# Optimization experiments

Measured on AMD Instinct MI355X. Metric: run time of the kernel, lower is better.

The kernel has to match this reference:

```python
import jax, jax.numpy as jnp
import numpy as np

N_NODES = 100000
N_EDGES = 1600000
IN_C, HID_C, OUT_C = 128, 128, 64


def setup_inputs() -> dict:
    key = jax.random.key(0)
    ks = jax.random.split(key, 8)
    x = jax.random.normal(ks[0], (N_NODES, IN_C), dtype=jnp.float32)
    edge_index = jax.random.randint(ks[1], (2, N_EDGES), 0, N_NODES, dtype=jnp.int32)
    # Glorot-ish init for GCNConv linear weights, zero bias (PyG default)
    def glorot(k, fan_in, fan_out):
        s = jnp.sqrt(6.0 / (fan_in + fan_out))
        return jax.random.uniform(k, (fan_in, fan_out), dtype=jnp.float32, minval=-s, maxval=s)
    return {
        "x": x,
        "edge_index": edge_index,
        "W1": glorot(ks[2], IN_C, HID_C), "b1": jnp.zeros((HID_C,), jnp.float32),
        "W2": glorot(ks[3], HID_C, HID_C), "b2": jnp.zeros((HID_C,), jnp.float32),
        "W3": glorot(ks[4], HID_C, OUT_C), "b3": jnp.zeros((OUT_C,), jnp.float32),
    }


def _gcn_norm(edge_index, num_nodes):
    # Add self-loops (PyG GCNConv default) and compute symmetric normalization
    loops = jnp.arange(num_nodes, dtype=edge_index.dtype)
    src = jnp.concatenate([edge_index[0], loops])  # [E+N]
    dst = jnp.concatenate([edge_index[1], loops])
    deg = jax.ops.segment_sum(jnp.ones_like(dst, dtype=jnp.float32), dst,
                              num_segments=num_nodes)
    deg_inv_sqrt = jnp.where(deg > 0, jax.lax.rsqrt(jnp.maximum(deg, 1.0)), 0.0)
    norm = deg_inv_sqrt[src] * deg_inv_sqrt[dst]  # [E+N]
    return src, dst, norm


def _gcn_layer(x, src, dst, norm, W, b, num_nodes):
    h = x @ W                                # [N, out] dense transform first
    msg = h[src] * norm[:, None]             # gather + scale  [E+N, out]
    out = jax.ops.segment_sum(msg, dst, num_segments=num_nodes)  # scatter-add
    return out + b


def reference(x, edge_index, W1, b1, W2, b2, W3, b3):
    n = x.shape[0]
    src, dst, norm = _gcn_norm(edge_index, n)
    h = jax.nn.relu(_gcn_layer(x, src, dst, norm, W1, b1, n))
    h = jax.nn.relu(_gcn_layer(h, src, dst, norm, W2, b2, n))
    return _gcn_layer(h, src, dst, norm, W3, b3, n)
```

## Files before the change

kernel.cpp:

```cpp
#include <hip/hip_runtime.h>

#define NN 100000
#define NE 1600000
#define NBK 391
#define BSH 8
#define MPAD 100096
#define SCB 391
#define CAP 5120

typedef unsigned short ushortT;
typedef unsigned long long ull;
using sh8 = __attribute__((ext_vector_type(8))) short;
using f4  = __attribute__((ext_vector_type(4))) float;


__device__ __forceinline__ unsigned short bfr(float f) {
  unsigned u = __float_as_uint(f);
  u += 0x7FFF + ((u >> 16) & 1);
  return (unsigned short)(u >> 16);
}
__device__ __forceinline__ float bf2f(unsigned short h) {
  return __uint_as_float(((unsigned)h) << 16);
}
__device__ __forceinline__ void acc8(const uint4 v, float* a) {
  a[0] += __uint_as_float(v.x << 16);
  a[1] += __uint_as_float(v.x & 0xFFFF0000u);
  a[2] += __uint_as_float(v.y << 16);
  a[3] += __uint_as_float(v.y & 0xFFFF0000u);
  a[4] += __uint_as_float(v.z << 16);
  a[5] += __uint_as_float(v.z & 0xFFFF0000u);
  a[6] += __uint_as_float(v.w << 16);
  a[7] += __uint_as_float(v.w & 0xFFFF0000u);
}
__device__ __forceinline__ sh8 hi8(const float4 a, const float4 b) {
  sh8 r;
  r[0] = (short)bfr(a.x); r[1] = (short)bfr(a.y);
  r[2] = (short)bfr(a.z); r[3] = (short)bfr(a.w);
  r[4] = (short)bfr(b.x); r[5] = (short)bfr(b.y);
  r[6] = (short)bfr(b.z); r[7] = (short)bfr(b.w);
  return r;
}


template <int COUT>
__device__ __forceinline__ void packone(const float* __restrict__ W,
                                        ushortT* __restrict__ Bp, int i) {
  const int j = i & 7;
  const int l = (i >> 3) & 63;
  const int rest = i >> 9;
  const int g = rest % (COUT / 16);
  const int ks = rest / (COUT / 16);
  const int k = (ks & 3) * 32 + (l >> 4) * 8 + j;
  const int n = g * 16 + (l & 15);
  const float v = W[k * COUT + n];
  const unsigned short h = bfr(v);
  Bp[i] = (ks < 4) ? h : bfr(v - bf2f(h));
}


__global__ __launch_bounds__(256) void k_scatterpack(
    const int* __restrict__ src, const int* __restrict__ dst,
    int* __restrict__ cursor, unsigned* __restrict__ pairArr,
    const float* __restrict__ W1, const float* __restrict__ W2,
    const float* __restrict__ W3, ushortT* __restrict__ Bp1,
    ushortT* __restrict__ Bp2, ushortT* __restrict__ Bp3) {
  if (blockIdx.x >= SCB) {
    const int i = (blockIdx.x - SCB) * 256 + threadIdx.x;
    if (i < 32768) packone<128>(W1, Bp1, i);
    else if (i < 65536) packone<128>(W2, Bp2, i - 32768);
    else packone<64>(W3, Bp3, i - 65536);
    return;
  }
  __shared__ int lcnt[512];
  __shared__ int lbase[512];
  __shared__ int lrank[NBK];
  __shared__ int bbase[NBK];
  __shared__ int sd2[256];
  __shared__ unsigned sorted[4096];
  __shared__ int target[4096];
  const int t = threadIdx.x;
  for (int i = t; i < 512; i += 256) lcnt[i] = 0;
  for (int i = t; i < NBK; i += 256) lrank[i] = 0;
  __syncthreads();
  const int base = blockIdx.x * 4096;
  int rs[16], rd[16];
#pragma unroll
  for (int q = 0; q < 16; q++) {
    int e = base + t + 256 * q;
    rs[q] = (e < NE) ? src[e] : -1;
    rd[q] = (e < NE) ? dst[e] : -1;
    if (rd[q] >= 0) atomicAdd(&lcnt[rd[q] >> BSH], 1);
  }
  __syncthreads();
  const int s0 = lcnt[2 * t];
  const int s1 = lcnt[2 * t + 1];
  sd2[t] = s0 + s1;
  __syncthreads();
  for (int off = 1; off < 256; off <<= 1) {
    int x = (t >= off) ? sd2[t - off] : 0;
    __syncthreads();
    sd2[t] += x;
    __syncthreads();
  }
  const int epair = sd2[t] - (s0 + s1);
  lbase[2 * t] = epair;
  lbase[2 * t + 1] = epair + s0;
  __syncthreads();
  for (int i = t; i < NBK; i += 256)
    if (lcnt[i] > 0) bbase[i] = atomicAdd(&cursor[i], lcnt[i]);
  __syncthreads();
#pragma unroll
  for (int q = 0; q < 16; q++) {
    if (rd[q] >= 0) {
      int b = rd[q] >> BSH;
      int r = atomicAdd(&lrank[b], 1);
      int slot = lbase[b] + r;
      sorted[slot] = ((unsigned)rs[q] << 8) | ((unsigned)rd[q] & 255u);
      target[slot] = b * CAP + bbase[b] + r;
    }
  }
  __syncthreads();
  const int n = min(4096, NE - base);
  for (int s = t; s < n; s += 256) pairArr[target[s]] = sorted[s];
}


__global__ __launch_bounds__(256) void k_buildcsr(const unsigned* __restrict__ pairArr,
                                                  const int* __restrict__ cnt,
                                                  float* __restrict__ dinv,
                                                  int* __restrict__ rowptr,
                                                  int* __restrict__ col) {
  __shared__ int lc[256];
  __shared__ int sd[256];
  __shared__ int bc[NBK];
  const int t = threadIdx.x;
  const int b = blockIdx.x;
  const int n0 = b << BSH;
  for (int i = t; i < NBK; i += 256) bc[i] = cnt[i];
  lc[t] = 0;
  __syncthreads();
  int partial = 0;
  for (int i = t; i < b; i += 256) partial += bc[i];
  sd[t] = partial;
  __syncthreads();
  for (int off = 128; off > 0; off >>= 1) {
    if (t < off) sd[t] += sd[t + off];
    __syncthreads();
  }
  const int ebeg = sd[0];
  const int myCnt = bc[b];
  __syncthreads();
  const unsigned* pb = pairArr + (size_t)b * CAP;
  for (int i = t; i < myCnt; i += 256)
    atomicAdd(&lc[pb[i] & 255u], 1);
  __syncthreads();
  const int v = lc[t];
  sd[t] = v;
  __syncthreads();
  for (int off = 1; off < 256; off <<= 1) {
    int x = (t >= off) ? sd[t - off] : 0;
    __syncthreads();
    sd[t] += x;
    __syncthreads();
  }
  const int excl = sd[t] - v;
  lc[t] = excl;
  const int node = n0 + t;
  if (node < NN) {
    rowptr[node] = ebeg + excl;
    dinv[node] = rsqrtf(1.0f + (float)v);
  }
  if (b == 0 && t == 0) rowptr[NN] = NE;
  __syncthreads();
  for (int i = t; i < myCnt; i += 256) {
    unsigned p = pb[i];
    int d = (int)(p & 255u);
    int srcv = (int)(p >> 8);
    int pos = atomicAdd(&lc[d], 1);
    col[ebeg + pos] = srcv;
  }
}


template <int COUT, bool FUSED>
__global__ __launch_bounds__(256) void k_gemmM(const ushortT* __restrict__ A,
                                               const float* __restrict__ X,
                                               const ushortT* __restrict__ Bp,
                                               const float* __restrict__ dinv,
                                               ushortT* __restrict__ hs) {
  constexpr int CGALL = COUT / 16;
  constexpr int RG = 2;
  constexpr int CG = 4;
  const int w = threadIdx.x >> 6;
  const int lane = threadIdx.x & 63;
  const int q = lane >> 4;
  const int c = lane & 15;
  int row0, cg0;
  if (COUT == 128) {
    row0 = blockIdx.x * 64 + (w & 1) * 32;
    cg0 = (w >> 1) * 4;
  } else {
    row0 = blockIdx.x * 128 + w * 32;
    cg0 = 0;
  }

  const ushortT* ap[RG];
  const float* xp[RG];
#pragma unroll
  for (int rg = 0; rg < RG; rg++) {
    const int row = row0 + rg * 16 + c;
    if (FUSED) xp[rg] = X + (size_t)min(row, NN - 1) * 128 + q * 8;
    else ap[rg] = A + (size_t)row * 128 + q * 8;
  }
  const ushortT* bp0 = Bp + (size_t)lane * 8;

  f4 acc[RG][CG];
#pragma unroll
  for (int i = 0; i < RG; i++)
#pragma unroll
    for (int j = 0; j < CG; j++) acc[i][j] = (f4){0.f, 0.f, 0.f, 0.f};

  sh8 ah[RG], bh[CG], bl[CG];
  sh8 nah[RG], nbh[CG], nbl[CG];

  auto loadA = [&](int kr, sh8 (&h)[RG]) {
#pragma unroll
    for (int rg = 0; rg < RG; rg++) {
      if (FUSED) {
        const float4 x0 = *reinterpret_cast<const float4*>(xp[rg] + kr * 32);
        const float4 x1 = *reinterpret_cast<const float4*>(xp[rg] + kr * 32 + 4);
        h[rg] = hi8(x0, x1);
      } else {
        h[rg] = *reinterpret_cast<const sh8*>(ap[rg] + kr * 32);
      }
    }
  };
  auto loadB = [&](int kr, sh8 (&h)[CG], sh8 (&l)[CG]) {
#pragma unroll
    for (int cg = 0; cg < CG; cg++) {
      h[cg] = *reinterpret_cast<const sh8*>(bp0 + (size_t)(kr * CGALL + cg0 + cg) * 512);
      l[cg] = *reinterpret_cast<const sh8*>(bp0 + (size_t)((4 + kr) * CGALL + cg0 + cg) * 512);
    }
  };

  loadA(0, ah);
  loadB(0, bh, bl);
#pragma unroll
  for (int kr = 0; kr < 4; kr++) {
    if (kr < 3) {
      loadA(kr + 1, nah);
      loadB(kr + 1, nbh, nbl);
    }
#pragma unroll
    for (int rg = 0; rg < RG; rg++)
#pragma unroll
      for (int cg = 0; cg < CG; cg++)
        acc[rg][cg] = __builtin_amdgcn_mfma_f32_16x16x32_bf16(ah[rg], bh[cg],
                                                              acc[rg][cg], 0, 0, 0);
#pragma unroll
    for (int rg = 0; rg < RG; rg++)
#pragma unroll
      for (int cg = 0; cg < CG; cg++)
        acc[rg][cg] = __builtin_amdgcn_mfma_f32_16x16x32_bf16(ah[rg], bl[cg],
                                                              acc[rg][cg], 0, 0, 0);
    if (kr < 3) {
#pragma unroll
      for (int rg = 0; rg < RG; rg++) ah[rg] = nah[rg];
#pragma unroll
      for (int cg = 0; cg < CG; cg++) { bh[cg] = nbh[cg]; bl[cg] = nbl[cg]; }
    }
  }

#pragma unroll
  for (int rg = 0; rg < RG; rg++) {
#pragma unroll
    for (int reg = 0; reg < 4; reg++) {
      const int row = row0 + rg * 16 + q * 4 + reg;
      if (row < NN) {
        const float dv = dinv[row];
#pragma unroll
        for (int cg = 0; cg < CG; cg++) {
          hs[(size_t)row * COUT + (cg0 + cg) * 16 + c] = bfr(acc[rg][cg][reg] * dv);
        }
      }
    }
  }
}


template <bool RELU>
__global__ __launch_bounds__(256) void k_agg128(const ushortT* __restrict__ hs,
                                                const int* __restrict__ rowptr,
                                                const int* __restrict__ col,
                                                const float* __restrict__ dinv,
                                                const float* __restrict__ bias,
                                                ushortT* __restrict__ A) {
  const int gid = blockIdx.x * 256 + threadIdx.x;
  const int node = gid >> 6;
  if (node >= NN) return;
  const int lane = threadIdx.x & 63;
  const int q = lane >> 4;
  const int chb = (lane & 15) * 8;
  const int beg = rowptr[node];
  const int end = rowptr[node + 1];

  float a[8] = {};
  if (q == 0) {
    const uint4 v = *reinterpret_cast<const uint4*>(hs + (long)node * 128 + chb);
    acc8(v, a);
  }

  int j = beg;
  if (j + 16 <= end) {
    int c0 = col[j + q];
    int c1 = col[j + 4 + q];
    int c2 = col[j + 8 + q];
    int c3 = col[j + 12 + q];
    while (true) {
      const uint4 v0 = *reinterpret_cast<const uint4*>(hs + (long)c0 * 128 + chb);
      const uint4 v1 = *reinterpret_cast<const uint4*>(hs + (long)c1 * 128 + chb);
      const uint4 v2 = *reinterpret_cast<const uint4*>(hs + (long)c2 * 128 + chb);
      const uint4 v3 = *reinterpret_cast<const uint4*>(hs + (long)c3 * 128 + chb);
      j += 16;
      const bool more = (j + 16 <= end);
      int n0, n1, n2, n3;
      if (more) {
        n0 = col[j + q]; n1 = col[j + 4 + q];
        n2 = col[j + 8 + q]; n3 = col[j + 12 + q];
      }
      acc8(v0, a);
      acc8(v1, a);
      acc8(v2, a);
      acc8(v3, a);
      if (!more) break;
      c0 = n0; c1 = n1; c2 = n2; c3 = n3;
    }
  }
  if (j + 8 <= end) {
    int c0 = col[j + q];
    int c1 = col[j + 4 + q];
    const uint4 v0 = *reinterpret_cast<const uint4*>(hs + (long)c0 * 128 + chb);
    const uint4 v1 = *reinterpret_cast<const uint4*>(hs + (long)c1 * 128 + chb);
    acc8(v0, a);
    acc8(v1, a);
    j += 8;
  }
  if (j + 4 <= end) {
    int c = col[j + q];
    const uint4 v = *reinterpret_cast<const uint4*>(hs + (long)c * 128 + chb);
    acc8(v, a);
    j += 4;
  }
  {
    const int r = end - j;
    if (q < r) {
      int c = col[j + q];
      const uint4 v = *reinterpret_cast<const uint4*>(hs + (long)c * 128 + chb);
      acc8(v, a);
    }
  }

#pragma unroll
  for (int i = 0; i < 8; i++) a[i] += __shfl(a[i], lane ^ 32);
#pragma unroll
  for (int i = 0; i < 8; i++) a[i] += __shfl(a[i], lane ^ 16);

  if (q == 0) {
    const float di = dinv[node];
    const float4 b0 = *reinterpret_cast<const float4*>(bias + chb);
    const float4 b1 = *reinterpret_cast<const float4*>(bias + chb + 4);
    float o[8];
    o[0] = fmaf(a[0], di, b0.x); o[1] = fmaf(a[1], di, b0.y);
    o[2] = fmaf(a[2], di, b0.z); o[3] = fmaf(a[3], di, b0.w);
    o[4] = fmaf(a[4], di, b1.x); o[5] = fmaf(a[5], di, b1.y);
    o[6] = fmaf(a[6], di, b1.z); o[7] = fmaf(a[7], di, b1.w);
    if (RELU) {
#pragma unroll
      for (int i = 0; i < 8; i++) o[i] = fmaxf(o[i], 0.f);
    }
    uint4 H;
    H.x = (unsigned)bfr(o[0]) | ((unsigned)bfr(o[1]) << 16);
    H.y = (unsigned)bfr(o[2]) | ((unsigned)bfr(o[3]) << 16);
    H.z = (unsigned)bfr(o[4]) | ((unsigned)bfr(o[5]) << 16);
    H.w = (unsigned)bfr(o[6]) | ((unsigned)bfr(o[7]) << 16);
    *reinterpret_cast<uint4*>(A + (long)node * 128 + chb) = H;
  }
}

__global__ __launch_bounds__(256) void k_agg64(const ushortT* __restrict__ hs,
                                               const int* __restrict__ rowptr,
                                               const int* __restrict__ col,
                                               const float* __restrict__ dinv,
                                               const float* __restrict__ bias,
                                               float* __restrict__ out) {
  const int gid = blockIdx.x * 256 + threadIdx.x;
  const int node = gid >> 6;
  if (node >= NN) return;
  const int lane = threadIdx.x & 63;
  const int o8 = lane >> 3;
  const int chb = (lane & 7) * 8;
  const int beg = rowptr[node];
  const int end = rowptr[node + 1];

  float a[8] = {};
  if (o8 == 0) {
    const uint4 v = *reinterpret_cast<const uint4*>(hs + (long)node * 64 + chb);
    acc8(v, a);
  }

  int j = beg;
  if (j + 16 <= end) {
    int c0 = col[j + o8];
    int c1 = col[j + 8 + o8];
    while (true) {
      const uint4 v0 = *reinterpret_cast<const uint4*>(hs + (long)c0 * 64 + chb);
      const uint4 v1 = *reinterpret_cast<const uint4*>(hs + (long)c1 * 64 + chb);
      j += 16;
      const bool more = (j + 16 <= end);
      int n0, n1;
      if (more) { n0 = col[j + o8]; n1 = col[j + 8 + o8]; }
      acc8(v0, a);
      acc8(v1, a);
      if (!more) break;
      c0 = n0; c1 = n1;
    }
  }
  for (; j + 8 <= end; j += 8) {
    int c = col[j + o8];
    const uint4 v = *reinterpret_cast<const uint4*>(hs + (long)c * 64 + chb);
    acc8(v, a);
  }
  {
    const int r = end - j;
    if (o8 < r) {
      int c = col[j + o8];
      const uint4 v = *reinterpret_cast<const uint4*>(hs + (long)c * 64 + chb);
      acc8(v, a);
    }
  }

#pragma unroll
  for (int i = 0; i < 8; i++) a[i] += __shfl(a[i], lane ^ 32);
#pragma unroll
  for (int i = 0; i < 8; i++) a[i] += __shfl(a[i], lane ^ 16);
#pragma unroll
  for (int i = 0; i < 8; i++) a[i] += __shfl(a[i], lane ^ 8);

  if (o8 == 0) {
    const float di = dinv[node];
    const float4 b0 = *reinterpret_cast<const float4*>(bias + chb);
    const float4 b1 = *reinterpret_cast<const float4*>(bias + chb + 4);
    float4 r0, r1;
    r0.x = fmaf(a[0], di, b0.x); r0.y = fmaf(a[1], di, b0.y);
    r0.z = fmaf(a[2], di, b0.z); r0.w = fmaf(a[3], di, b0.w);
    r1.x = fmaf(a[4], di, b1.x); r1.y = fmaf(a[5], di, b1.y);
    r1.z = fmaf(a[6], di, b1.z); r1.w = fmaf(a[7], di, b1.w);
    *reinterpret_cast<float4*>(out + (long)node * 64 + chb) = r0;
    *reinterpret_cast<float4*>(out + (long)node * 64 + chb + 4) = r1;
  }
}


extern "C" void kernel_launch(void* const* d_in, const int* in_sizes, int n_in,
                              void* d_out, int out_size, void* d_ws, size_t ws_size,
                              hipStream_t stream) {
  const float* x  = (const float*)d_in[0];
  const int* ei   = (const int*)d_in[1];
  const float* W1 = (const float*)d_in[2];
  const float* b1 = (const float*)d_in[3];
  const float* W2 = (const float*)d_in[4];
  const float* b2 = (const float*)d_in[5];
  const float* W3 = (const float*)d_in[6];
  const float* b3 = (const float*)d_in[7];
  float* out = (float*)d_out;
  const int* srcp = ei;
  const int* dstp = ei + NE;

  char* wsb = (char*)d_ws;
  size_t off = 0;
  auto alloc = [&](size_t bytes) -> void* {
    void* p = wsb + off;
    off += (bytes + 255) & ~(size_t)255;
    return p;
  };
  ushortT* A   = (ushortT*)alloc((size_t)MPAD * 128 * 2);
  ushortT* hs  = (ushortT*)alloc((size_t)NN * 128 * 2);
  int*   col    = (int*)alloc((size_t)NE * 4);
  int*   rowptr = (int*)alloc((size_t)(NN + 1) * 4);
  float* dinv   = (float*)alloc((size_t)NN * 4);
  int*   cursor = (int*)alloc((size_t)NBK * 4);
  ushortT* Bp1 = (ushortT*)alloc((size_t)32768 * 2);
  ushortT* Bp2 = (ushortT*)alloc((size_t)32768 * 2);
  ushortT* Bp3 = (ushortT*)alloc((size_t)16384 * 2);
  unsigned* pairArr = (unsigned*)hs;
  (void)ws_size; (void)in_sizes; (void)n_in; (void)out_size;

  hipMemsetAsync(cursor, 0, (size_t)NBK * 4, stream);
  k_scatterpack<<<SCB + 320, 256, 0, stream>>>(srcp, dstp, cursor, pairArr,
                                               W1, W2, W3, Bp1, Bp2, Bp3);
  k_buildcsr<<<NBK, 256, 0, stream>>>(pairArr, cursor, dinv, rowptr, col);

  const int aggGrid = (NN * 64) / 256;
  const int gemmGrid128 = MPAD / 64;
  const int gemmGrid64 = MPAD / 128;

  k_gemmM<128, true><<<gemmGrid128, 256, 0, stream>>>(nullptr, x, Bp1, dinv, hs);
  k_agg128<true><<<aggGrid, 256, 0, stream>>>(hs, rowptr, col, dinv, b1, A);
  k_gemmM<128, false><<<gemmGrid128, 256, 0, stream>>>(A, nullptr, Bp2, dinv, hs);
  k_agg128<true><<<aggGrid, 256, 0, stream>>>(hs, rowptr, col, dinv, b2, A);
  k_gemmM<64, false><<<gemmGrid64, 256, 0, stream>>>(A, nullptr, Bp3, dinv, hs);
  k_agg64<<<aggGrid, 256, 0, stream>>>(hs, rowptr, col, dinv, b3, out);
}
```

Before: 366.9 us.

## Fuse neighbor aggregation with the next layer's GEMM via shared-memory tile

Replaces the separate aggregation kernel and the following MFMA GEMM with one kernel. Each block aggregates 64 nodes, writes the post-ReLU bf16 rows into a swizzled LDS tile, then multiplies that tile by the packed weights and writes the scaled result. This removes the round trip of the intermediate activation matrix A through global memory and two kernel launches. In exchange, each wave processes 16 nodes serially with a shallower unroll, so latency hiding for the irregular gathers may drop.

Result: slower. 386.7 us (+5.4%).

```diff
diff --git a/kernel.cpp b/kernel.cpp
--- a/kernel.cpp
+++ b/kernel.cpp
@@ -7,6 +7,7 @@
 #define MPAD 100096
 #define SCB 391
 #define CAP 5120
+#define NB64 1563
 
 typedef unsigned short ushortT;
 typedef unsigned long long ull;
@@ -288,104 +289,128 @@
 }
 
 
-template <bool RELU>
-__global__ __launch_bounds__(256) void k_agg128(const ushortT* __restrict__ hs,
-                                                const int* __restrict__ rowptr,
-                                                const int* __restrict__ col,
-                                                const float* __restrict__ dinv,
-                                                const float* __restrict__ bias,
-                                                ushortT* __restrict__ A) {
-  const int gid = blockIdx.x * 256 + threadIdx.x;
-  const int node = gid >> 6;
-  if (node >= NN) return;
-  const int lane = threadIdx.x & 63;
+template <int COUT>
+__global__ __launch_bounds__(256) void k_aggemm(
+    const ushortT* __restrict__ hs_in, const int* __restrict__ rowptr,
+    const int* __restrict__ col, const float* __restrict__ dinv,
+    const float* __restrict__ bias, const ushortT* __restrict__ Bp,
+    ushortT* __restrict__ hs_out) {
+  constexpr int CGALL = COUT / 16;
+  __shared__ ushortT At[64 * 128];
+  const int t = threadIdx.x;
+  const int w = t >> 6;
+  const int lane = t & 63;
   const int q = lane >> 4;
-  const int chb = (lane & 15) * 8;
-  const int beg = rowptr[node];
-  const int end = rowptr[node + 1];
-
-  float a[8] = {};
-  if (q == 0) {
-    const uint4 v = *reinterpret_cast<const uint4*>(hs + (long)node * 128 + chb);
-    acc8(v, a);
-  }
-
-  int j = beg;
-  if (j + 16 <= end) {
-    int c0 = col[j + q];
-    int c1 = col[j + 4 + q];
-    int c2 = col[j + 8 + q];
-    int c3 = col[j + 12 + q];
-    while (true) {
-      const uint4 v0 = *reinterpret_cast<const uint4*>(hs + (long)c0 * 128 + chb);
-      const uint4 v1 = *reinterpret_cast<const uint4*>(hs + (long)c1 * 128 + chb);
-      const uint4 v2 = *reinterpret_cast<const uint4*>(hs + (long)c2 * 128 + chb);
-      const uint4 v3 = *reinterpret_cast<const uint4*>(hs + (long)c3 * 128 + chb);
-      j += 16;
-      const bool more = (j + 16 <= end);
-      int n0, n1, n2, n3;
-      if (more) {
-        n0 = col[j + q]; n1 = col[j + 4 + q];
-        n2 = col[j + 8 + q]; n3 = col[j + 12 + q];
+  const int c = lane & 15;
+  const int chb = c * 8;
+  const int n0 = blockIdx.x * 64;
+
+  for (int it = 0; it < 16; ++it) {
+    const int r = w * 16 + it;
+    const int node = n0 + r;
+    float a[8] = {};
+    if (node < NN) {
+      const int beg = rowptr[node];
+      const int end = rowptr[node + 1];
+      if (q == 0) {
+        const uint4 v = *reinterpret_cast<const uint4*>(hs_in + (long)node * 128 + chb);
+        acc8(v, a);
       }
-      acc8(v0, a);
-      acc8(v1, a);
-      acc8(v2, a);
-      acc8(v3, a);
-      if (!more) break;
-      c0 = n0; c1 = n1; c2 = n2; c3 = n3;
-    }
-  }
-  if (j + 8 <= end) {
-    int c0 = col[j + q];
-    int c1 = col[j + 4 + q];
-    const uint4 v0 = *reinterpret_cast<const uint4*>(hs + (long)c0 * 128 + chb);
-    const uint4 v1 = *reinterpret_cast<const uint4*>(hs + (long)c1 * 128 + chb);
-    acc8(v0, a);
-    acc8(v1, a);
-    j += 8;
-  }
-  if (j + 4 <= end) {
-    int c = col[j + q];
-    const uint4 v = *reinterpret_cast<const uint4*>(hs + (long)c * 128 + chb);
-    acc8(v, a);
-    j += 4;
-  }
-  {
-    const int r = end - j;
-    if (q < r) {
-      int c = col[j + q];
-      const uint4 v = *reinterpret_cast<const uint4*>(hs + (long)c * 128 + chb);
-      acc8(v, a);
-    }
-  }
-
-#pragma unroll
-  for (int i = 0; i < 8; i++) a[i] += __shfl(a[i], lane ^ 32);
-#pragma unroll
-  for (int i = 0; i < 8; i++) a[i] += __shfl(a[i], lane ^ 16);
-
-  if (q == 0) {
-    const float di = dinv[node];
-    const float4 b0 = *reinterpret_cast<const float4*>(bias + chb);
-    const float4 b1 = *reinterpret_cast<const float4*>(bias + chb + 4);
-    float o[8];
-    o[0] = fmaf(a[0], di, b0.x); o[1] = fmaf(a[1], di, b0.y);
-    o[2] = fmaf(a[2], di, b0.z); o[3] = fmaf(a[3], di, b0.w);
-    o[4] = fmaf(a[4], di, b1.x); o[5] = fmaf(a[5], di, b1.y);
-    o[6] = fmaf(a[6], di, b1.z); o[7] = fmaf(a[7], di, b1.w);
-    if (RELU) {
+      int j = beg;
+      if (j + 8 <= end) {
+        int c0 = col[j + q];
+        int c1 = col[j + 4 + q];
+        while (true) {
+          const uint4 v0 = *reinterpret_cast<const uint4*>(hs_in + (long)c0 * 128 + chb);
+          const uint4 v1 = *reinterpret_cast<const uint4*>(hs_in + (long)c1 * 128 + chb);
+          j += 8;
+          const bool more = (j + 8 <= end);
+          int m0, m1;
+          if (more) { m0 = col[j + q]; m1 = col[j + 4 + q]; }
+          acc8(v0, a);
+          acc8(v1, a);
+          if (!more) break;
+          c0 = m0; c1 = m1;
+        }
+      }
+      if (j + 4 <= end) {
+        int cc = col[j + q];
+        const uint4 v = *reinterpret_cast<const uint4*>(hs_in + (long)cc * 128 + chb);
+        acc8(v, a);
+        j += 4;
+      }
+      {
+        const int rem = end - j;
+        if (q < rem) {
+          int cc = col[j + q];
+          const uint4 v = *reinterpret_cast<const uint4*>(hs_in + (long)cc * 128 + chb);
+          acc8(v, a);
+        }
+      }
+    }
+#pragma unroll
+    for (int i = 0; i < 8; i++) a[i] += __shfl(a[i], lane ^ 32);
+#pragma unroll
+    for (int i = 0; i < 8; i++) a[i] += __shfl(a[i], lane ^ 16);
+    if (q == 0 && node < NN) {
+      const float di = dinv[node];
+      const float4 b0 = *reinterpret_cast<const float4*>(bias + chb);
+      const float4 b1 = *reinterpret_cast<const float4*>(bias + chb + 4);
+      float o[8];
+      o[0] = fmaf(a[0], di, b0.x); o[1] = fmaf(a[1], di, b0.y);
+      o[2] = fmaf(a[2], di, b0.z); o[3] = fmaf(a[3], di, b0.w);
+      o[4] = fmaf(a[4], di, b1.x); o[5] = fmaf(a[5], di, b1.y);
+      o[6] = fmaf(a[6], di, b1.z); o[7] = fmaf(a[7], di, b1.w);
 #pragma unroll
       for (int i = 0; i < 8; i++) o[i] = fmaxf(o[i], 0.f);
-    }
-    uint4 H;
-    H.x = (unsigned)bfr(o[0]) | ((unsigned)bfr(o[1]) << 16);
-    H.y = (unsigned)bfr(o[2]) | ((unsigned)bfr(o[3]) << 16);
-    H.z = (unsigned)bfr(o[4]) | ((unsigned)bfr(o[5]) << 16);
-    H.w = (unsigned)bfr(o[6]) | ((unsigned)bfr(o[7]) << 16);
-    *reinterpret_cast<uint4*>(A + (long)node * 128 + chb) = H;
-  }
-}
+      uint4 H;
+      H.x = (unsigned)bfr(o[0]) | ((unsigned)bfr(o[1]) << 16);
+      H.y = (unsigned)bfr(o[2]) | ((unsigned)bfr(o[3]) << 16);
+      H.z = (unsigned)bfr(o[4]) | ((unsigned)bfr(o[5]) << 16);
+      H.w = (unsigned)bfr(o[6]) | ((unsigned)bfr(o[7]) << 16);
+      const unsigned bo = (unsigned)(r * 256 + c * 16) ^ (unsigned)((r & 7) << 4);
+      *reinterpret_cast<uint4*>(reinterpret_cast<char*>(At) + bo) = H;
+    }
+  }
+  __syncthreads();
+
+  f4 acc[CGALL];
+#pragma unroll
+  for (int cg = 0; cg < CGALL; ++cg) acc[cg] = (f4){0.f, 0.f, 0.f, 0.f};
+  const ushortT* bp0 = Bp + (size_t)lane * 8;
+  const int arow = w * 16 + c;
+  const char* ab = reinterpret_cast<const char*>(At);
+#pragma unroll
+  for (int kr = 0; kr < 4; ++kr) {
+    const unsigned bo =
+        (unsigned)(arow * 256 + kr * 64 + q * 16) ^ (unsigned)((arow & 7) << 4);
+    const sh8 af = *reinterpret_cast<const sh8*>(ab + bo);
+    sh8 bh[CGALL];
+#pragma unroll
+    for (int cg = 0; cg < CGALL; ++cg)
+      bh[cg] = *reinterpret_cast<const sh8*>(bp0 + (size_t)(kr * CGALL + cg) * 512);
+#pragma unroll
+    for (int cg = 0; cg < CGALL; ++cg)
+      acc[cg] = __builtin_amdgcn_mfma_f32_16x16x32_bf16(af, bh[cg], acc[cg], 0, 0, 0);
+#pragma unroll
+    for (int cg = 0; cg < CGALL; ++cg)
+      bh[cg] = *reinterpret_cast<const sh8*>(bp0 + (size_t)((4 + kr) * CGALL + cg) * 512);
+#pragma unroll
+    for (int cg = 0; cg < CGALL; ++cg)
+      acc[cg] = __builtin_amdgcn_mfma_f32_16x16x32_bf16(af, bh[cg], acc[cg], 0, 0, 0);
+  }
+#pragma unroll
+  for (int reg = 0; reg < 4; ++reg) {
+    const int row = n0 + w * 16 + q * 4 + reg;
+    if (row < NN) {
+      const float dv = dinv[row];
+#pragma unroll
+      for (int cg = 0; cg < CGALL; ++cg)
+        hs_out[(size_t)row * COUT + cg * 16 + c] = bfr(acc[cg][reg] * dv);
+    }
+  }
+}
+
 
 __global__ __launch_bounds__(256) void k_agg64(const ushortT* __restrict__ hs,
                                                const int* __restrict__ rowptr,
@@ -483,8 +508,8 @@
     off += (bytes + 255) & ~(size_t)255;
     return p;
   };
-  ushortT* A   = (ushortT*)alloc((size_t)MPAD * 128 * 2);
-  ushortT* hs  = (ushortT*)alloc((size_t)NN * 128 * 2);
+  ushortT* hs1 = (ushortT*)alloc((size_t)MPAD * 128 * 2);
+  ushortT* hs2 = (ushortT*)alloc((size_t)NN * 128 * 2);
   int*   col    = (int*)alloc((size_t)NE * 4);
   int*   rowptr = (int*)alloc((size_t)(NN + 1) * 4);
   float* dinv   = (float*)alloc((size_t)NN * 4);
@@ -492,7 +517,8 @@
   ushortT* Bp1 = (ushortT*)alloc((size_t)32768 * 2);
   ushortT* Bp2 = (ushortT*)alloc((size_t)32768 * 2);
   ushortT* Bp3 = (ushortT*)alloc((size_t)16384 * 2);
-  unsigned* pairArr = (unsigned*)hs;
+  unsigned* pairArr = (unsigned*)hs2;
+  ushortT* hs3 = hs1;
   (void)ws_size; (void)in_sizes; (void)n_in; (void)out_size;
 
   hipMemsetAsync(cursor, 0, (size_t)NBK * 4, stream);
@@ -502,12 +528,9 @@
 
   const int aggGrid = (NN * 64) / 256;
   const int gemmGrid128 = MPAD / 64;
-  const int gemmGrid64 = MPAD / 128;
-
-  k_gemmM<128, true><<<gemmGrid128, 256, 0, stream>>>(nullptr, x, Bp1, dinv, hs);
-  k_agg128<true><<<aggGrid, 256, 0, stream>>>(hs, rowptr, col, dinv, b1, A);
-  k_gemmM<128, false><<<gemmGrid128, 256, 0, stream>>>(A, nullptr, Bp2, dinv, hs);
-  k_agg128<true><<<aggGrid, 256, 0, stream>>>(hs, rowptr, col, dinv, b2, A);
-  k_gemmM<64, false><<<gemmGrid64, 256, 0, stream>>>(A, nullptr, Bp3, dinv, hs);
-  k_agg64<<<aggGrid, 256, 0, stream>>>(hs, rowptr, col, dinv, b3, out);
-}
+
+  k_gemmM<128, true><<<gemmGrid128, 256, 0, stream>>>(nullptr, x, Bp1, dinv, hs1);
+  k_aggemm<128><<<NB64, 256, 0, stream>>>(hs1, rowptr, col, dinv, b1, Bp2, hs2);
+  k_aggemm<64><<<NB64, 256, 0, stream>>>(hs2, rowptr, col, dinv, b2, Bp3, hs3);
+  k_agg64<<<aggGrid, 256, 0, stream>>>(hs3, rowptr, col, dinv, b3, out);
+}
```
